# Optimization experiments

Measured on AMD Instinct MI355X. Metric: run time of the kernel, lower is better.

Reference implementation:

```python
import jax, jax.numpy as jnp
import numpy as np

NUM_HEADS = 16

def setup_inputs() -> dict:
    key = jax.random.key(0)
    ks = jax.random.split(key, 11)
    B, S, D = 4, 1024, 1024
    M = 128
    hd = D // NUM_HEADS
    s = 0.02
    return {
        'x':  jax.random.normal(ks[0], (B, S, D), jnp.float32),
        'Wq': jax.random.normal(ks[1], (D, D), jnp.float32) * s,
        'bq': jax.random.normal(ks[2], (D,), jnp.float32) * s,
        'Wk': jax.random.normal(ks[3], (D, D), jnp.float32) * s,
        'bk': jax.random.normal(ks[4], (D,), jnp.float32) * s,
        'Wv': jax.random.normal(ks[5], (D, D), jnp.float32) * s,
        'bv': jax.random.normal(ks[6], (D,), jnp.float32) * s,
        'Wo': jax.random.normal(ks[7], (D, D), jnp.float32) * s,
        'bo': jax.random.normal(ks[8], (D,), jnp.float32) * s,
        'rel_k': jax.random.normal(ks[9], (2 * M + 1, hd), jnp.float32),
        'rel_v': jax.random.normal(ks[10], (2 * M + 1, hd), jnp.float32),
    }

def reference(x, Wq, bq, Wk, bk, Wv, bv, Wo, bo, rel_k, rel_v):
    B, S, D = x.shape
    H = NUM_HEADS
    hd = D // H
    M = (rel_k.shape[0] - 1) // 2

    def proj(W, b):
        # torch nn.Linear: x @ W.T + b, then split heads -> [B,H,S,hd]
        return (x @ W.T + b).reshape(B, S, H, hd).transpose(0, 2, 1, 3)

    q = proj(Wq, bq)
    k = proj(Wk, bk)
    v = proj(Wv, bv)

    # relative position index matrix [S,S]: clip(j - i, -M, M) + M
    r = jnp.arange(S)
    idx = jnp.clip(r[None, :] - r[:, None], -M, M) + M
    rpk = rel_k[idx]  # [S,S,hd] (equivalent to one-hot matmul lookup)
    rpv = rel_v[idx]  # [S,S,hd]

    content = jnp.einsum('bhqd,bhkd->bhqk', q, k)
    relative = jnp.einsum('bhqd,qkd->bhqk', q, rpk)
    scores = (content + relative) / jnp.sqrt(jnp.float32(hd))
    w = jax.nn.softmax(scores, axis=-1)  # [B,H,S,S]

    out = jnp.einsum('bhqk,bhkd->bhqd', w, v) + jnp.einsum('bhqk,qkd->bhqd', w, rpv)
    out = out.transpose(0, 2, 1, 3).reshape(B, S, D)
    return out @ Wo.T + bo
```

## Files before the change

kernel.cpp:

```cpp
#include <hip/hip_runtime.h>
#include <hip/hip_bf16.h>
#include <math.h>

#define SEQ 1024
#define NH 16
#define HD 64
#define DM 1024
#define MWIN 128
#define RR 257

typedef __attribute__((ext_vector_type(8))) short bf16x8;
typedef __attribute__((ext_vector_type(4))) float f32x4;

__device__ __forceinline__ unsigned short f2b_bits(float f) {
  return __builtin_bit_cast(unsigned short, __float2bfloat16(f));
}
__device__ __forceinline__ float b2f(unsigned short u) {
  return __uint_as_float(((unsigned int)u) << 16);
}
__device__ __forceinline__ void gl16(const void* g, void* l) {
  __builtin_amdgcn_global_load_lds(
      (const __attribute__((address_space(1))) unsigned int*)g,
      (__attribute__((address_space(3))) unsigned int*)l, 16, 0, 0);
}

__global__ __launch_bounds__(256) void f2b_kernel(const float* __restrict__ in,
                                                  unsigned short* __restrict__ out,
                                                  int n4) {
  int i = blockIdx.x * 256 + threadIdx.x;
  const int stride = gridDim.x * 256;
  for (; i < n4; i += stride) {
    float4 v = ((const float4*)in)[i];
    ushort4 o;
    o.x = f2b_bits(v.x); o.y = f2b_bits(v.y); o.z = f2b_bits(v.z); o.w = f2b_bits(v.w);
    ((ushort4*)out)[i] = o;
  }
}

__global__ __launch_bounds__(256) void w4_conv(const float* __restrict__ w0,
                                               const float* __restrict__ w1,
                                               const float* __restrict__ w2,
                                               const float* __restrict__ w3,
                                               unsigned short* __restrict__ out) {
  int idx = blockIdx.x * 256 + threadIdx.x;
  const int m = idx >> 18, local = idx & 262143;
  const float* src = m == 0 ? w0 : (m == 1 ? w1 : (m == 2 ? w2 : w3));
  float4 v = ((const float4*)src)[local];
  ushort4 o;
  o.x = f2b_bits(v.x); o.y = f2b_bits(v.y); o.z = f2b_bits(v.z); o.w = f2b_bits(v.w);
  ((ushort4*)out)[idx] = o;
}

__global__ __launch_bounds__(256) void relk_conv(const float* __restrict__ rk,
                                                 unsigned short* __restrict__ out) {
  int idx = blockIdx.x * 256 + threadIdx.x;
  int r = idx >> 6;
  int rs = r > 256 ? 256 : r;
  out[idx] = f2b_bits(rk[rs * HD + (idx & 63)]);
}

__global__ __launch_bounds__(256) void relv_t(const float* __restrict__ rv,
                                              unsigned short* __restrict__ out) {
  int idx = blockIdx.x * 256 + threadIdx.x;
  if (idx >= 64 * 288) return;
  int d = idx / 288, r = idx % 288;
  out[idx] = (r < RR) ? f2b_bits(rv[(size_t)r * HD + d]) : (unsigned short)0;
}

__global__ __launch_bounds__(256) void qkv_gemm(const unsigned short* __restrict__ A,
                                                const unsigned short* __restrict__ Bw,
                                                const float* __restrict__ bq,
                                                const float* __restrict__ bk,
                                                const float* __restrict__ bv,
                                                unsigned short* __restrict__ Qo,
                                                unsigned short* __restrict__ Ko,
                                                unsigned short* __restrict__ Vo) {
  __shared__ unsigned short As[128 * 32];
  __shared__ unsigned short Bs[128 * 32];
  const int t = threadIdx.x;
  const int lane = t & 63;
  const int wave = t >> 6;
  const int wr = wave >> 1, wc = wave & 1;
  const int lrow = lane & 15, lk = lane >> 4;
  const int m0 = blockIdx.x * 128, n0 = blockIdx.y * 128;

  const int mat = n0 >> 10;
  const float* bias = mat == 0 ? bq : (mat == 1 ? bk : bv);
  unsigned short* Co = mat == 0 ? Qo : (mat == 1 ? Ko : Vo);
  const float scale = mat == 0 ? 0.125f : 1.0f;

  const unsigned short* Ag = A + (size_t)m0 * DM;
  const unsigned short* Bg = Bw + (size_t)n0 * DM;
  const int r0 = t >> 2, r1 = (t + 256) >> 2;
  const int c0 = (t & 3) << 3;

  f32x4 acc[4][4] = {};

  for (int k0 = 0; k0 < DM; k0 += 32) {
    __syncthreads();
    gl16(Ag + (size_t)r0 * DM + k0 + c0, &As[t * 8]);
    gl16(Bg + (size_t)r0 * DM + k0 + c0, &Bs[t * 8]);
    gl16(Ag + (size_t)r1 * DM + k0 + c0, &As[(t + 256) * 8]);
    gl16(Bg + (size_t)r1 * DM + k0 + c0, &Bs[(t + 256) * 8]);
    __syncthreads();
    bf16x8 af[4], bfr[4];
#pragma unroll
    for (int i = 0; i < 4; ++i)
      af[i] = *(const bf16x8*)&As[(wr * 64 + i * 16 + lrow) * 32 + lk * 8];
#pragma unroll
    for (int j = 0; j < 4; ++j)
      bfr[j] = *(const bf16x8*)&Bs[(wc * 64 + j * 16 + lrow) * 32 + lk * 8];
#pragma unroll
    for (int i = 0; i < 4; ++i)
#pragma unroll
      for (int j = 0; j < 4; ++j)
        acc[i][j] = __builtin_amdgcn_mfma_f32_16x16x32_bf16(af[i], bfr[j], acc[i][j], 0, 0, 0);
  }

  float bvv[4];
#pragma unroll
  for (int j = 0; j < 4; ++j) bvv[j] = bias[(n0 & 1023) + wc * 64 + j * 16 + lrow];

#pragma unroll
  for (int i = 0; i < 4; ++i) {
#pragma unroll
    for (int j = 0; j < 4; ++j) {
      const int nl = (n0 & 1023) + wc * 64 + j * 16 + lrow;
      const int h = nl >> 6, d = nl & 63;
#pragma unroll
      for (int r = 0; r < 4; ++r) {
        const int m = m0 + wr * 64 + i * 16 + lk * 4 + r;
        const int b = m >> 10, s = m & 1023;
        float v = (acc[i][j][r] + bvv[j]) * scale;
        Co[((size_t)(b * NH + h) * SEQ + s) * HD + d] = f2b_bits(v);
      }
    }
  }
}

template<int MODE>
__global__ __launch_bounds__(256) void mfma_gemm(const unsigned short* __restrict__ A,
                                                 const unsigned short* __restrict__ B,
                                                 const float* __restrict__ bias,
                                                 float* __restrict__ Cf,
                                                 unsigned short* __restrict__ Cb,
                                                 int K) {
  __shared__ unsigned short As[128 * 32];
  __shared__ unsigned short Bs[128 * 32];
  const int t = threadIdx.x;
  const int lane = t & 63;
  const int wave = t >> 6;
  const int wr = wave >> 1, wc = wave & 1;
  const int lrow = lane & 15, lk = lane >> 4;
  const int m0 = blockIdx.x * 128, n0 = blockIdx.y * 128;

  const unsigned short* Ag = A + (size_t)m0 * K;
  const unsigned short* Bg = B + (size_t)n0 * K;
  const int r0 = t >> 2, r1 = (t + 256) >> 2;
  const int c0 = (t & 3) << 3;

  f32x4 acc[4][4] = {};

  for (int k0 = 0; k0 < K; k0 += 32) {
    __syncthreads();
    gl16(Ag + (size_t)r0 * K + k0 + c0, &As[t * 8]);
    gl16(Bg + (size_t)r0 * K + k0 + c0, &Bs[t * 8]);
    gl16(Ag + (size_t)r1 * K + k0 + c0, &As[(t + 256) * 8]);
    gl16(Bg + (size_t)r1 * K + k0 + c0, &Bs[(t + 256) * 8]);
    __syncthreads();
    bf16x8 af[4], bfr[4];
#pragma unroll
    for (int i = 0; i < 4; ++i)
      af[i] = *(const bf16x8*)&As[(wr * 64 + i * 16 + lrow) * 32 + lk * 8];
#pragma unroll
    for (int j = 0; j < 4; ++j)
      bfr[j] = *(const bf16x8*)&Bs[(wc * 64 + j * 16 + lrow) * 32 + lk * 8];
#pragma unroll
    for (int i = 0; i < 4; ++i)
#pragma unroll
      for (int j = 0; j < 4; ++j)
        acc[i][j] = __builtin_amdgcn_mfma_f32_16x16x32_bf16(af[i], bfr[j], acc[i][j], 0, 0, 0);
  }

  float bvv[4];
  if (MODE == 1) {
#pragma unroll
    for (int j = 0; j < 4; ++j) bvv[j] = bias[n0 + wc * 64 + j * 16 + lrow];
  }
#pragma unroll
  for (int i = 0; i < 4; ++i) {
#pragma unroll
    for (int j = 0; j < 4; ++j) {
      const int n = n0 + wc * 64 + j * 16 + lrow;
#pragma unroll
      for (int r = 0; r < 4; ++r) {
        const int m = m0 + wr * 64 + i * 16 + lk * 4 + r;
        float v = acc[i][j][r];
        if (MODE == 1) {
          Cf[(size_t)m * DM + n] = v + bvv[j];
        } else {
          if (n < RR) Cb[(size_t)m * RR + n] = f2b_bits(v);
        }
      }
    }
  }
}

__global__ __launch_bounds__(256) void flash_mfma(
    const unsigned short* __restrict__ Qb,
    const unsigned short* __restrict__ Kb,
    const unsigned short* __restrict__ Vb,
    const unsigned short* __restrict__ qrb,
    const unsigned short* __restrict__ relvT,
    unsigned short* __restrict__ attnb) {
  __shared__ unsigned short Ks[64 * 64];
  __shared__ unsigned short VT[64][72];
  __shared__ unsigned short Ps[4][16][72];
  __shared__ unsigned short wrs[64][288];

  const int t = threadIdx.x;
  const int lane = t & 63;
  const int w = t >> 6;
  const int lq = lane & 15;
  const int g  = lane >> 4;
  const int bh = blockIdx.y;
  const int q0 = blockIdx.x * 64;
  const int qw0 = q0 + w * 16;

  const unsigned short* Qp = Qb + (size_t)bh * SEQ * HD;
  const unsigned short* Kp = Kb + (size_t)bh * SEQ * HD;
  const unsigned short* Vp = Vb + (size_t)bh * SEQ * HD;

  {
    unsigned int* wz = (unsigned int*)wrs;
    for (int i = t; i < 64 * 288 / 2; i += 256) wz[i] = 0u;
  }

  bf16x8 aq[2];
  aq[0] = *(const bf16x8*)(Qp + (size_t)(qw0 + lq) * HD + g * 8);
  aq[1] = *(const bf16x8*)(Qp + (size_t)(qw0 + lq) * HD + 32 + g * 8);

  const size_t qrow0 = ((size_t)bh * SEQ + qw0 + g * 4) * RR;
  float bq0[4], bq256[4];
#pragma unroll
  for (int rr = 0; rr < 4; ++rr) {
    bq0[rr]   = b2f(qrb[qrow0 + (size_t)rr * RR]);
    bq256[rr] = b2f(qrb[qrow0 + (size_t)rr * RR + 256]);
  }

  float l[4] = {}, accL[4] = {}, accR[4] = {};
  f32x4 out1[4] = {};

  const int sv = (t & 31) * 2;
  const int dv = (t >> 5) * 8;
  bf16x8 v0 = *(const bf16x8*)(Vp + (size_t)sv * HD + dv);
  bf16x8 v1 = *(const bf16x8*)(Vp + (size_t)(sv + 1) * HD + dv);

  const int c1 = t + 256;
  const int src0 = ((t >> 3) << 3) | ((t & 7) ^ ((t >> 3) & 7));
  const int src1 = ((c1 >> 3) << 3) | ((c1 & 7) ^ ((c1 >> 3) & 7));

  for (int kt = 0; kt < 16; ++kt) {
    const int k0 = kt * 64;
    __syncthreads();
    gl16(Kp + (size_t)k0 * HD + src0 * 8, &Ks[t * 8]);
    gl16(Kp + (size_t)k0 * HD + src1 * 8, &Ks[(t + 256) * 8]);
#pragma unroll
    for (int j = 0; j < 8; ++j) {
      unsigned int pv = (unsigned short)v0[j] | ((unsigned int)(unsigned short)v1[j] << 16);
      *(unsigned int*)&VT[dv + j][sv] = pv;
    }
    if (kt < 15) {
      v0 = *(const bf16x8*)(Vp + (size_t)(k0 + 64 + sv) * HD + dv);
      v1 = *(const bf16x8*)(Vp + (size_t)(k0 + 64 + sv + 1) * HD + dv);
    }

    const int diag = k0 - qw0;
    float bias[4][4];
    if (diag <= -192) {
#pragma unroll
      for (int j = 0; j < 4; ++j)
#pragma unroll
        for (int rr = 0; rr < 4; ++rr) bias[j][rr] = bq0[rr];
    } else if (diag >= 144) {
#pragma unroll
      for (int j = 0; j < 4; ++j)
#pragma unroll
        for (int rr = 0; rr < 4; ++rr) bias[j][rr] = bq256[rr];
    } else {
      const int dbase = diag + lq - g * 4;
#pragma unroll
      for (int j = 0; j < 4; ++j)
#pragma unroll
        for (int rr = 0; rr < 4; ++rr) {
          int delta = dbase + j * 16 - rr;
          int r = delta < -MWIN ? 0 : (delta > MWIN ? 256 : delta + MWIN);
          bias[j][rr] = b2f(qrb[qrow0 + (size_t)rr * RR + r]);
        }
    }
    __syncthreads();

    f32x4 sc[4] = {};
#pragma unroll
    for (int j = 0; j < 4; ++j) {
      const int row = j * 16 + lq;
#pragma unroll
      for (int kk = 0; kk < 2; ++kk) {
        const int ch = (kk * 4 + g) ^ (row & 7);
        bf16x8 bk = *(const bf16x8*)&Ks[row * 64 + ch * 8];
        sc[j] = __builtin_amdgcn_mfma_f32_16x16x32_bf16(aq[kk], bk, sc[j], 0, 0, 0);
      }
    }

    float wvf[4][4], ssum[4] = {};
#pragma unroll
    for (int j = 0; j < 4; ++j)
#pragma unroll
      for (int rr = 0; rr < 4; ++rr) {
        float wv = __expf(sc[j][rr] + bias[j][rr]);
        wvf[j][rr] = wv;
        ssum[rr] += wv;
      }
#pragma unroll
    for (int rr = 0; rr < 4; ++rr) {
#pragma unroll
      for (int o = 1; o < 16; o <<= 1) ssum[rr] += __shfl_xor(ssum[rr], o);
      l[rr] += ssum[rr];
    }

    const int dbase = diag + lq - g * 4;
#pragma unroll
    for (int j = 0; j < 4; ++j)
#pragma unroll
      for (int rr = 0; rr < 4; ++rr) {
        const unsigned short ub = f2b_bits(wvf[j][rr]);
        Ps[w][g * 4 + rr][j * 16 + lq] = ub;
        const int delta = dbase + j * 16 - rr;
        if (delta <= -MWIN)      accL[rr] += wvf[j][rr];
        else if (delta >= MWIN)  accR[rr] += wvf[j][rr];
        else                     wrs[w * 16 + g * 4 + rr][delta + MWIN] = ub;
      }

    bf16x8 pa[2];
    pa[0] = *(const bf16x8*)&Ps[w][lq][g * 8];
    pa[1] = *(const bf16x8*)&Ps[w][lq][32 + g * 8];
#pragma unroll
    for (int jd = 0; jd < 4; ++jd) {
      const int vrow = jd * 16 + lq;
#pragma unroll
      for (int kk = 0; kk < 2; ++kk) {
        bf16x8 vb = *(const bf16x8*)&VT[vrow][kk * 32 + g * 8];
        out1[jd] = __builtin_amdgcn_mfma_f32_16x16x32_bf16(pa[kk], vb, out1[jd], 0, 0, 0);
      }
    }
  }

#pragma unroll
  for (int rr = 0; rr < 4; ++rr) {
    float sL = accL[rr], sR = accR[rr];
#pragma unroll
    for (int o = 1; o < 16; o <<= 1) { sL += __shfl_xor(sL, o); sR += __shfl_xor(sR, o); }
    if (lq == 0) {
      wrs[w * 16 + g * 4 + rr][0]   = f2b_bits(sL);
      wrs[w * 16 + g * 4 + rr][256] = f2b_bits(sR);
    }
  }
  __syncthreads();

  f32x4 out2[4] = {};
#pragma unroll
  for (int kk = 0; kk < 9; ++kk) {
    bf16x8 pa2 = *(const bf16x8*)&wrs[w * 16 + lq][kk * 32 + g * 8];
#pragma unroll
    for (int jd = 0; jd < 4; ++jd) {
      bf16x8 vb = *(const bf16x8*)(relvT + (size_t)(jd * 16 + lq) * 288 + kk * 32 + g * 8);
      out2[jd] = __builtin_amdgcn_mfma_f32_16x16x32_bf16(pa2, vb, out2[jd], 0, 0, 0);
    }
  }

  const int b = bh >> 4, h = bh & 15;
#pragma unroll
  for (int jd = 0; jd < 4; ++jd)
#pragma unroll
    for (int rr = 0; rr < 4; ++rr) {
      const int s = qw0 + g * 4 + rr;
      const int d = jd * 16 + lq;
      float vout = (out1[jd][rr] + out2[jd][rr]) / l[rr];
      attnb[(size_t)(b * SEQ + s) * DM + h * HD + d] = f2b_bits(vout);
    }
}

extern "C" void kernel_launch(void* const* d_in, const int* in_sizes, int n_in,
                              void* d_out, int out_size, void* d_ws, size_t ws_size,
                              hipStream_t stream) {
  const float* x     = (const float*)d_in[0];
  const float* Wq    = (const float*)d_in[1];
  const float* bq    = (const float*)d_in[2];
  const float* Wk    = (const float*)d_in[3];
  const float* bk    = (const float*)d_in[4];
  const float* Wv    = (const float*)d_in[5];
  const float* bv    = (const float*)d_in[6];
  const float* Wo    = (const float*)d_in[7];
  const float* bo    = (const float*)d_in[8];
  const float* rel_k = (const float*)d_in[9];
  const float* rel_v = (const float*)d_in[10];
  float* out = (float*)d_out;

  unsigned short* us    = (unsigned short*)d_ws;
  unsigned short* qrb   = us;
  unsigned short* xb    = us + 16842752;
  unsigned short* attnb = xb;
  unsigned short* Wqb   = xb + 4194304;
  unsigned short* Wob   = Wqb + 3145728;
  unsigned short* Qbf   = Wob + 1048576;
  unsigned short* Kbb   = Qbf + 4194304;
  unsigned short* Vbb   = Kbb + 4194304;
  unsigned short* relkb = Vbb + 4194304;
  unsigned short* relvtb= relkb + 24576;

  f2b_kernel<<<2048, 256, 0, stream>>>(x, xb, 1048576);
  w4_conv<<<4096, 256, 0, stream>>>(Wq, Wk, Wv, Wo, Wqb);
  relk_conv<<<96, 256, 0, stream>>>(rel_k, relkb);
  relv_t<<<72, 256, 0, stream>>>(rel_v, relvtb);

  qkv_gemm<<<dim3(32, 24), 256, 0, stream>>>(xb, Wqb, bq, bk, bv, Qbf, Kbb, Vbb);

  mfma_gemm<2><<<dim3(512, 3), 256, 0, stream>>>(Qbf, relkb, nullptr, nullptr, qrb, HD);

  flash_mfma<<<dim3(16, 64), 256, 0, stream>>>(Qbf, Kbb, Vbb, qrb, relvtb, attnb);

  mfma_gemm<1><<<dim3(32, 8), 256, 0, stream>>>(attnb, Wob, bo, out, nullptr, DM);
}
```

Baseline: 261.2 us.

## Process 128-key tiles per iteration in flash attention and skip bias lookups off-band

The flash kernel's key loop now stages 128 keys of K and V per iteration instead of 64, halving the number of barrier-separated iterations. Each iteration processes two 64-key halves. Halves entirely outside the relative-position window use a constant bias and sum probabilities straight into the edge accumulators, skipping per-element index tests and scattered LDS writes. LDS moves to dynamic shared memory of about 80 KB, which may lower the number of blocks resident per CU.

New measurement: 249.6 us. 4.4% less time.

```diff
diff --git a/kernel.cpp b/kernel.cpp
--- a/kernel.cpp
+++ b/kernel.cpp
@@ -206,6 +206,8 @@
   }
 }
 
+#define FLASH_LDS_BYTES 80896
+
 __global__ __launch_bounds__(256) void flash_mfma(
     const unsigned short* __restrict__ Qb,
     const unsigned short* __restrict__ Kb,
@@ -213,10 +215,11 @@
     const unsigned short* __restrict__ qrb,
     const unsigned short* __restrict__ relvT,
     unsigned short* __restrict__ attnb) {
-  __shared__ unsigned short Ks[64 * 64];
-  __shared__ unsigned short VT[64][72];
-  __shared__ unsigned short Ps[4][16][72];
-  __shared__ unsigned short wrs[64][288];
+  extern __shared__ char smem[];
+  unsigned short* Ks = (unsigned short*)smem;
+  unsigned short (*VT)[144]    = (unsigned short(*)[144])(smem + 16384);
+  unsigned short (*Ps)[16][72] = (unsigned short(*)[16][72])(smem + 34816);
+  unsigned short (*wrs)[288]   = (unsigned short(*)[288])(smem + 44032);
 
   const int t = threadIdx.x;
   const int lane = t & 63;
@@ -232,8 +235,8 @@
   const unsigned short* Vp = Vb + (size_t)bh * SEQ * HD;
 
   {
-    unsigned int* wz = (unsigned int*)wrs;
-    for (int i = t; i < 64 * 288 / 2; i += 256) wz[i] = 0u;
+    unsigned int* wz = (unsigned int*)(smem + 44032);
+    for (int i = t; i < 9216; i += 256) wz[i] = 0u;
   }
 
   bf16x8 aq[2];
@@ -251,106 +254,142 @@
   float l[4] = {}, accL[4] = {}, accR[4] = {};
   f32x4 out1[4] = {};
 
-  const int sv = (t & 31) * 2;
-  const int dv = (t >> 5) * 8;
-  bf16x8 v0 = *(const bf16x8*)(Vp + (size_t)sv * HD + dv);
-  bf16x8 v1 = *(const bf16x8*)(Vp + (size_t)(sv + 1) * HD + dv);
-
-  const int c1 = t + 256;
-  const int src0 = ((t >> 3) << 3) | ((t & 7) ^ ((t >> 3) & 7));
-  const int src1 = ((c1 >> 3) << 3) | ((c1 & 7) ^ ((c1 >> 3) & 7));
-
-  for (int kt = 0; kt < 16; ++kt) {
-    const int k0 = kt * 64;
-    __syncthreads();
-    gl16(Kp + (size_t)k0 * HD + src0 * 8, &Ks[t * 8]);
-    gl16(Kp + (size_t)k0 * HD + src1 * 8, &Ks[(t + 256) * 8]);
+  const int p = lane;
+  const int dvv = w * 16;
+  bf16x8 v00 = *(const bf16x8*)(Vp + (size_t)(2 * p) * HD + dvv);
+  bf16x8 v01 = *(const bf16x8*)(Vp + (size_t)(2 * p) * HD + dvv + 8);
+  bf16x8 v10 = *(const bf16x8*)(Vp + (size_t)(2 * p + 1) * HD + dvv);
+  bf16x8 v11 = *(const bf16x8*)(Vp + (size_t)(2 * p + 1) * HD + dvv + 8);
+
+  for (int kt = 0; kt < 8; ++kt) {
+    const int k0 = kt * 128;
+    __syncthreads();
+
+#pragma unroll
+    for (int u = 0; u < 4; ++u) {
+      const int ch = t + u * 256;
+      const int row = ch >> 3;
+      const int src = (row << 3) | ((ch & 7) ^ (row & 7));
+      gl16(Kp + (size_t)k0 * HD + src * 8, &Ks[ch * 8]);
+    }
 #pragma unroll
     for (int j = 0; j < 8; ++j) {
-      unsigned int pv = (unsigned short)v0[j] | ((unsigned int)(unsigned short)v1[j] << 16);
-      *(unsigned int*)&VT[dv + j][sv] = pv;
-    }
-    if (kt < 15) {
-      v0 = *(const bf16x8*)(Vp + (size_t)(k0 + 64 + sv) * HD + dv);
-      v1 = *(const bf16x8*)(Vp + (size_t)(k0 + 64 + sv + 1) * HD + dv);
-    }
-
-    const int diag = k0 - qw0;
-    float bias[4][4];
-    if (diag <= -192) {
-#pragma unroll
-      for (int j = 0; j < 4; ++j)
-#pragma unroll
-        for (int rr = 0; rr < 4; ++rr) bias[j][rr] = bq0[rr];
-    } else if (diag >= 144) {
-#pragma unroll
-      for (int j = 0; j < 4; ++j)
-#pragma unroll
-        for (int rr = 0; rr < 4; ++rr) bias[j][rr] = bq256[rr];
-    } else {
-      const int dbase = diag + lq - g * 4;
+      *(unsigned int*)&VT[dvv + j][2 * p] =
+          (unsigned short)v00[j] | ((unsigned int)(unsigned short)v10[j] << 16);
+      *(unsigned int*)&VT[dvv + 8 + j][2 * p] =
+          (unsigned short)v01[j] | ((unsigned int)(unsigned short)v11[j] << 16);
+    }
+
+    const int dh0 = k0 - qw0, dh1 = dh0 + 64;
+    const int cls0 = dh0 <= -192 ? 0 : (dh0 >= 144 ? 1 : 2);
+    const int cls1 = dh1 <= -192 ? 0 : (dh1 >= 144 ? 1 : 2);
+    float bias0[4][4], bias1[4][4];
+    if (cls0 == 2) {
+      const int dbase = dh0 + lq - g * 4;
 #pragma unroll
       for (int j = 0; j < 4; ++j)
 #pragma unroll
         for (int rr = 0; rr < 4; ++rr) {
           int delta = dbase + j * 16 - rr;
           int r = delta < -MWIN ? 0 : (delta > MWIN ? 256 : delta + MWIN);
-          bias[j][rr] = b2f(qrb[qrow0 + (size_t)rr * RR + r]);
-        }
-    }
-    __syncthreads();
-
-    f32x4 sc[4] = {};
-#pragma unroll
-    for (int j = 0; j < 4; ++j) {
-      const int row = j * 16 + lq;
-#pragma unroll
-      for (int kk = 0; kk < 2; ++kk) {
-        const int ch = (kk * 4 + g) ^ (row & 7);
-        bf16x8 bk = *(const bf16x8*)&Ks[row * 64 + ch * 8];
-        sc[j] = __builtin_amdgcn_mfma_f32_16x16x32_bf16(aq[kk], bk, sc[j], 0, 0, 0);
-      }
-    }
-
-    float wvf[4][4], ssum[4] = {};
-#pragma unroll
-    for (int j = 0; j < 4; ++j)
+          bias0[j][rr] = b2f(qrb[qrow0 + (size_t)rr * RR + r]);
+        }
+    }
+    if (cls1 == 2) {
+      const int dbase = dh1 + lq - g * 4;
+#pragma unroll
+      for (int j = 0; j < 4; ++j)
+#pragma unroll
+        for (int rr = 0; rr < 4; ++rr) {
+          int delta = dbase + j * 16 - rr;
+          int r = delta < -MWIN ? 0 : (delta > MWIN ? 256 : delta + MWIN);
+          bias1[j][rr] = b2f(qrb[qrow0 + (size_t)rr * RR + r]);
+        }
+    }
+    __syncthreads();
+
+    if (kt < 7) {
+      const unsigned short* Vn = Vp + (size_t)(k0 + 128) * HD + dvv;
+      v00 = *(const bf16x8*)(Vn + (size_t)(2 * p) * HD);
+      v01 = *(const bf16x8*)(Vn + (size_t)(2 * p) * HD + 8);
+      v10 = *(const bf16x8*)(Vn + (size_t)(2 * p + 1) * HD);
+      v11 = *(const bf16x8*)(Vn + (size_t)(2 * p + 1) * HD + 8);
+    }
+
+#pragma unroll
+    for (int h = 0; h < 2; ++h) {
+      const int dh = h == 0 ? dh0 : dh1;
+      const int cls = h == 0 ? cls0 : cls1;
+      const float (*bias)[4] = h == 0 ? bias0 : bias1;
+
+      f32x4 sc[4] = {};
+#pragma unroll
+      for (int j = 0; j < 4; ++j) {
+        const int row = h * 64 + j * 16 + lq;
+#pragma unroll
+        for (int kk = 0; kk < 2; ++kk) {
+          const int ch = (kk * 4 + g) ^ (lq & 7);
+          bf16x8 bk = *(const bf16x8*)&Ks[row * 64 + ch * 8];
+          sc[j] = __builtin_amdgcn_mfma_f32_16x16x32_bf16(aq[kk], bk, sc[j], 0, 0, 0);
+        }
+      }
+
+      float wvf[4][4], ssum[4] = {};
+      if (cls == 2) {
+#pragma unroll
+        for (int j = 0; j < 4; ++j)
+#pragma unroll
+          for (int rr = 0; rr < 4; ++rr) {
+            float wv = __expf(sc[j][rr] + bias[j][rr]);
+            wvf[j][rr] = wv; ssum[rr] += wv;
+          }
+        const int dbase = dh + lq - g * 4;
+#pragma unroll
+        for (int j = 0; j < 4; ++j)
+#pragma unroll
+          for (int rr = 0; rr < 4; ++rr) {
+            const unsigned short ub = f2b_bits(wvf[j][rr]);
+            Ps[w][g * 4 + rr][j * 16 + lq] = ub;
+            const int delta = dbase + j * 16 - rr;
+            if (delta <= -MWIN)      accL[rr] += wvf[j][rr];
+            else if (delta >= MWIN)  accR[rr] += wvf[j][rr];
+            else                     wrs[w * 16 + g * 4 + rr][delta + MWIN] = ub;
+          }
+      } else {
+        const float* bb = cls == 0 ? bq0 : bq256;
+#pragma unroll
+        for (int j = 0; j < 4; ++j)
+#pragma unroll
+          for (int rr = 0; rr < 4; ++rr) {
+            float wv = __expf(sc[j][rr] + bb[rr]);
+            wvf[j][rr] = wv; ssum[rr] += wv;
+            Ps[w][g * 4 + rr][j * 16 + lq] = f2b_bits(wv);
+          }
+#pragma unroll
+        for (int rr = 0; rr < 4; ++rr) {
+          if (cls == 0) accL[rr] += ssum[rr]; else accR[rr] += ssum[rr];
+        }
+      }
+
 #pragma unroll
       for (int rr = 0; rr < 4; ++rr) {
-        float wv = __expf(sc[j][rr] + bias[j][rr]);
-        wvf[j][rr] = wv;
-        ssum[rr] += wv;
-      }
-#pragma unroll
-    for (int rr = 0; rr < 4; ++rr) {
-#pragma unroll
-      for (int o = 1; o < 16; o <<= 1) ssum[rr] += __shfl_xor(ssum[rr], o);
-      l[rr] += ssum[rr];
-    }
-
-    const int dbase = diag + lq - g * 4;
-#pragma unroll
-    for (int j = 0; j < 4; ++j)
-#pragma unroll
-      for (int rr = 0; rr < 4; ++rr) {
-        const unsigned short ub = f2b_bits(wvf[j][rr]);
-        Ps[w][g * 4 + rr][j * 16 + lq] = ub;
-        const int delta = dbase + j * 16 - rr;
-        if (delta <= -MWIN)      accL[rr] += wvf[j][rr];
-        else if (delta >= MWIN)  accR[rr] += wvf[j][rr];
-        else                     wrs[w * 16 + g * 4 + rr][delta + MWIN] = ub;
-      }
-
-    bf16x8 pa[2];
-    pa[0] = *(const bf16x8*)&Ps[w][lq][g * 8];
-    pa[1] = *(const bf16x8*)&Ps[w][lq][32 + g * 8];
-#pragma unroll
-    for (int jd = 0; jd < 4; ++jd) {
-      const int vrow = jd * 16 + lq;
-#pragma unroll
-      for (int kk = 0; kk < 2; ++kk) {
-        bf16x8 vb = *(const bf16x8*)&VT[vrow][kk * 32 + g * 8];
-        out1[jd] = __builtin_amdgcn_mfma_f32_16x16x32_bf16(pa[kk], vb, out1[jd], 0, 0, 0);
+        float s0 = ssum[rr];
+#pragma unroll
+        for (int o = 1; o < 16; o <<= 1) s0 += __shfl_xor(s0, o);
+        l[rr] += s0;
+      }
+
+      bf16x8 pa[2];
+      pa[0] = *(const bf16x8*)&Ps[w][lq][g * 8];
+      pa[1] = *(const bf16x8*)&Ps[w][lq][32 + g * 8];
+#pragma unroll
+      for (int jd = 0; jd < 4; ++jd) {
+        const int vrow = jd * 16 + lq;
+#pragma unroll
+        for (int kk = 0; kk < 2; ++kk) {
+          bf16x8 vb = *(const bf16x8*)&VT[vrow][h * 64 + kk * 32 + g * 8];
+          out1[jd] = __builtin_amdgcn_mfma_f32_16x16x32_bf16(pa[kk], vb, out1[jd], 0, 0, 0);
+        }
       }
     }
   }
@@ -427,7 +466,10 @@
 
   mfma_gemm<2><<<dim3(512, 3), 256, 0, stream>>>(Qbf, relkb, nullptr, nullptr, qrb, HD);
 
-  flash_mfma<<<dim3(16, 64), 256, 0, stream>>>(Qbf, Kbb, Vbb, qrb, relvtb, attnb);
+  (void)hipFuncSetAttribute(reinterpret_cast<const void*>(flash_mfma),
+                            hipFuncAttributeMaxDynamicSharedMemorySize,
+                            FLASH_LDS_BYTES);
+  flash_mfma<<<dim3(16, 64), 256, FLASH_LDS_BYTES, stream>>>(Qbf, Kbb, Vbb, qrb, relvtb, attnb);
 
   mfma_gemm<1><<<dim3(32, 8), 256, 0, stream>>>(attnb, Wob, bo, out, nullptr, DM);
 }
```
